# Optimization experiments

Measured on AMD Instinct MI355X. Metric: run time of the kernel, lower is better.

The kernel has to match this reference:

```python
import jax, jax.numpy as jnp
import numpy as np

DIM = 512
L = 4096
B, H, W = 8, 64, 64
EPS = 1e-06
BN_EPS = 1e-05


def setup_inputs() -> dict:
    key = jax.random.key(0)
    ks = jax.random.split(key, 16)
    s = 1.0 / np.sqrt(DIM)
    d = {
        'x': jax.random.normal(ks[0], (B, DIM, H, W), dtype=jnp.float32),
        'pos_emb': jax.random.normal(ks[1], (1, L, DIM), dtype=jnp.float32),
        'Wq': jax.random.uniform(ks[2], (DIM, DIM), jnp.float32, -s, s),
        'bq': jax.random.uniform(ks[3], (DIM,), jnp.float32, -s, s),
        'Wk': jax.random.uniform(ks[4], (DIM, DIM), jnp.float32, -s, s),
        'bk': jax.random.uniform(ks[5], (DIM,), jnp.float32, -s, s),
        'Wv': jax.random.uniform(ks[6], (DIM, DIM), jnp.float32, -s, s),
        'bv': jax.random.uniform(ks[7], (DIM,), jnp.float32, -s, s),
        'Wq1': jax.random.uniform(ks[8], (DIM, DIM), jnp.float32, -s, s),
        'bq1': jax.random.uniform(ks[9], (DIM,), jnp.float32, -s, s),
        'Wk1': jax.random.uniform(ks[10], (DIM, DIM), jnp.float32, -s, s),
        'bk1': jax.random.uniform(ks[11], (DIM,), jnp.float32, -s, s),
        'gamma': jax.random.normal(ks[12], (1,), jnp.float32) * 0.1,
        'bn_weight': jnp.ones((DIM,), jnp.float32),
        'bn_bias': jnp.zeros((DIM,), jnp.float32),
    }
    return d


def reference(x, pos_emb, Wq, bq, Wk, bk, Wv, bv, Wq1, bq1, Wk1, bk1, gamma, bn_weight, bn_bias):
    Bb, C, Hh, Ww = x.shape
    # [B,C,H,W] -> [B, L, C] tokens
    xs = x.transpose(0, 2, 3, 1).reshape(Bb, Hh * Ww, C) + pos_emb
    Q = jax.nn.relu(xs @ Wq.T + bq)   # kernel_fun = ReLU
    K = jax.nn.relu(xs @ Wk.T + bk)
    V = xs @ Wv.T + bv
    Q1 = xs @ Wq1.T + bq1
    K1 = xs @ Wk1.T + bk1
    # torch einsum 'blc,bcc,bl->blc' uses only diag(KV); compute it directly:
    # diagKV[b,c] = sum_l K[b,l,c] * V[b,l,c]
    diagKV = jnp.einsum('blc,blc->bc', K, V)
    Ksum = K.sum(axis=1)  # == K^T summed over last axis, [B,C]
    Z = 1.0 / jnp.einsum('blc,bc->bl', Q, Ksum + EPS)
    result = Q * diagKV[:, None, :] * Z[:, :, None]  # [B,L,C]
    # channel-softmax attention: softmax over last dim of Q1^T @ K1, [B,C,C]
    mid = jax.nn.softmax(jnp.einsum('blc,bld->bcd', Q1, K1), axis=-1)
    result = result @ mid  # [B,L,C]
    xs = xs + gamma * result
    y = xs.transpose(0, 2, 1).reshape(Bb, C, Hh, Ww)
    # BatchNorm2d in training mode (fresh module): batch stats, biased variance
    mean = y.mean(axis=(0, 2, 3))
    var = y.var(axis=(0, 2, 3))
    yn = (y - mean[None, :, None, None]) * jax.lax.rsqrt(var + BN_EPS)[None, :, None, None]
    yn = yn * bn_weight[None, :, None, None] + bn_bias[None, :, None, None]
    return jax.nn.relu(yn)
```

## Files before the change

### kernel.cpp

```cpp
#include <hip/hip_runtime.h>
#include <stdint.h>

typedef float f32x4 __attribute__((ext_vector_type(4)));
typedef short bf16x8 __attribute__((ext_vector_type(8)));

__device__ __forceinline__ float bf2f(unsigned short h){
  union { unsigned int u; float f; } v; v.u = ((unsigned int)h) << 16; return v.f;
}
__device__ __forceinline__ unsigned short f2bf(float f){
  union { float f; unsigned int u; } v; v.f = f;
  return (unsigned short)((v.u + 0x7fffu + ((v.u >> 16) & 1u)) >> 16);
}

typedef __attribute__((address_space(1))) const unsigned int ga_u32;
typedef __attribute__((address_space(3))) unsigned int ls_u32;
__device__ __forceinline__ void async_load16(const void* g, void* l){
  __builtin_amdgcn_global_load_lds((ga_u32*)g, (ls_u32*)l, 16, 0, 0);
}

#define CFENCE() asm volatile("" ::: "memory")
#define SB0() __builtin_amdgcn_sched_barrier(0)

__global__ __launch_bounds__(256) void k_prep_w(
    const float* __restrict__ w0, const float* __restrict__ w1,
    const float* __restrict__ w2, const float* __restrict__ w3,
    const float* __restrict__ w4, unsigned short* __restrict__ out)
{
  int i = blockIdx.x * 256 + threadIdx.x;
  const float* w = (blockIdx.y == 0) ? w0 : (blockIdx.y == 1) ? w1 :
                   (blockIdx.y == 2) ? w2 : (blockIdx.y == 3) ? w3 : w4;
  out[(size_t)blockIdx.y * 262144 + i] = f2bf(w[i]);
}
__global__ __launch_bounds__(256) void k_prep_b(
    const float* __restrict__ b0, const float* __restrict__ b1,
    const float* __restrict__ b2, const float* __restrict__ b3,
    const float* __restrict__ b4, float* __restrict__ out)
{
  int i = blockIdx.x * 256 + threadIdx.x;
  int s = i >> 9, r = i & 511;
  const float* b = (s == 0) ? b0 : (s == 1) ? b1 : (s == 2) ? b2 : (s == 3) ? b3 : b4;
  out[i] = b[r];
}

__global__ __launch_bounds__(256) void k_build_xs(
    const float* __restrict__ x, const float* __restrict__ pos,
    unsigned short* __restrict__ xsb)
{
  __shared__ float tile[64][65];
  const int lt = blockIdx.x, ct = blockIdx.y;
  const int t = threadIdx.x;
  const int rr = t >> 3, c8 = (t & 7) * 8;
  float pr[16];
  #pragma unroll
  for (int pass = 0; pass < 2; pass++){
    int gl = lt*64 + rr + pass*32;
    f32x4 p0 = *(const f32x4*)(pos + (size_t)gl * 512 + ct*64 + c8);
    f32x4 p1 = *(const f32x4*)(pos + (size_t)gl * 512 + ct*64 + c8 + 4);
    #pragma unroll
    for (int s = 0; s < 4; s++){ pr[pass*8+s] = p0[s]; pr[pass*8+4+s] = p1[s]; }
  }
  for (int b = 0; b < 8; b++){
    #pragma unroll
    for (int pass = 0; pass < 2; pass++){
      int r = rr + pass * 32;
      const float* src = x + ((size_t)b * 512 + ct*64 + r) * 4096 + lt*64 + c8;
      f32x4 v0 = *(const f32x4*)src;
      f32x4 v1 = *(const f32x4*)(src + 4);
      #pragma unroll
      for (int s = 0; s < 4; s++){ tile[r][c8+s] = v0[s]; tile[r][c8+4+s] = v1[s]; }
    }
    __syncthreads();
    #pragma unroll
    for (int pass = 0; pass < 2; pass++){
      int ll = rr + pass * 32;
      int gl = lt*64 + ll;
      bf16x8 hv;
      #pragma unroll
      for (int s = 0; s < 8; s++)
        hv[s] = (short)f2bf(tile[c8+s][ll] + pr[pass*8+s]);
      *(bf16x8*)(xsb + ((size_t)b * 4096 + gl) * 512 + ct*64 + c8) = hv;
    }
    __syncthreads();
  }
}

__global__ __launch_bounds__(256) void k_softmax_t(
    const float* __restrict__ S0, const float* __restrict__ S1,
    const float* __restrict__ diag, unsigned short* __restrict__ midT)
{
  __shared__ unsigned short tr[64 * 514];
  const int it = blockIdx.x, z = blockIdx.y;
  const int t = threadIdx.x;
  const int lane = t & 63, w = t >> 6;
  for (int rr = 0; rr < 16; rr++){
    int i = rr*4 + w;
    size_t rowo = (size_t)z * 262144 + (size_t)(it*64 + i) * 512 + lane*8;
    const float* p0 = S0 + rowo;
    const float* p1 = S1 + rowo;
    f32x4 v0 = *(const f32x4*)p0 + *(const f32x4*)p1;
    f32x4 v1 = *(const f32x4*)(p0 + 4) + *(const f32x4*)(p1 + 4);
    float mx = v0[0];
    #pragma unroll
    for (int s = 1; s < 4; s++) mx = fmaxf(mx, v0[s]);
    #pragma unroll
    for (int s = 0; s < 4; s++) mx = fmaxf(mx, v1[s]);
    #pragma unroll
    for (int m = 1; m < 64; m <<= 1) mx = fmaxf(mx, __shfl_xor(mx, m));
    float e[8]; float sum = 0.f;
    #pragma unroll
    for (int s = 0; s < 4; s++){ e[s]   = __expf(v0[s] - mx); sum += e[s]; }
    #pragma unroll
    for (int s = 0; s < 4; s++){ e[4+s] = __expf(v1[s] - mx); sum += e[4+s]; }
    #pragma unroll
    for (int m = 1; m < 64; m <<= 1) sum += __shfl_xor(sum, m);
    float sc = diag[z*512 + it*64 + i] / sum;
    #pragma unroll
    for (int s = 0; s < 8; s++) tr[i*514 + lane*8 + s] = f2bf(e[s] * sc);
  }
  __syncthreads();
  for (int ps = 0; ps < 16; ps++){
    int j = ps*32 + (t >> 3);
    int i0 = (t & 7) * 8;
    bf16x8 hv;
    #pragma unroll
    for (int s = 0; s < 8; s++) hv[s] = (short)tr[(i0+s)*514 + j];
    *(bf16x8*)(midT + ((size_t)z*512 + j)*512 + it*64 + i0) = hv;
  }
}

#define GEMM_PRE()                                                            \
  const int tid = threadIdx.x;                                                \
  const int lane = tid & 63;                                                  \
  const int wave = tid >> 6;                                                  \
  const int wm = wave >> 1, wn = wave & 1;                                    \
  size_t aoff[4], boff[4]; int ldsq[4];                                       \
  _Pragma("unroll")                                                           \
  for (int i = 0; i < 4; i++){                                                \
    int qq = i*4 + wave;                                                      \
    int ch = qq*64 + lane;                                                    \
    int m  = ch >> 3, p = ch & 7;                                             \
    int lc = p ^ (m & 7);                                                     \
    aoff[i] = (size_t)(m0 + m) * K + lc*8;                                    \
    boff[i] = (size_t)m * K + lc*8;                                           \
    ldsq[i] = qq * 1024;                                                      \
  }                                                                           \
  f32x4 acc[4][4];                                                            \
  const f32x4 vzero = {0.f,0.f,0.f,0.f};                                      \
  _Pragma("unroll")                                                           \
  for (int i = 0; i < 4; i++)                                                 \
    _Pragma("unroll")                                                         \
    for (int j = 0; j < 4; j++) acc[i][j] = vzero;                            \
  int arow[4], brow[4];                                                       \
  _Pragma("unroll")                                                           \
  for (int f = 0; f < 4; f++){                                                \
    arow[f] = (wm*64 + f*16 + (lane & 15)) * 64;                              \
    brow[f] = (wn*64 + f*16 + (lane & 15)) * 64;                              \
  }                                                                           \
  const int kg = lane >> 4;                                                   \
  const int l7 = lane & 7;                                                    \
  const int l15 = lane & 15;

#define GEMM_STAGE2(buf, kt, BB)                                              \
  _Pragma("unroll")                                                           \
  for (int i = 0; i < 4; i++){                                                \
    async_load16(Ae + aoff[i] + (kt)*64, (char*)&smem[(buf)*8192] + ldsq[i]); \
    async_load16((BB) + boff[i] + (kt)*64, (char*)&smem[16384 + (buf)*8192] + ldsq[i]); \
  }

#define GEMM_COMPUTE2(buf, ACC)                                               \
  _Pragma("unroll")                                                           \
  for (int ks = 0; ks < 2; ks++){                                             \
    bf16x8 a[4], b[4];                                                        \
    const int pa = (ks*4 + kg) ^ l7;                                          \
    _Pragma("unroll")                                                         \
    for (int f = 0; f < 4; f++){                                              \
      a[f] = *(const bf16x8*)&smem[(buf)*8192 + arow[f] + pa*8];              \
      b[f] = *(const bf16x8*)&smem[16384 + (buf)*8192 + brow[f] + pa*8];      \
    }                                                                         \
    _Pragma("unroll")                                                         \
    for (int i = 0; i < 4; i++)                                               \
      _Pragma("unroll")                                                       \
      for (int j = 0; j < 4; j++)                                             \
        (ACC)[i][j] = __builtin_amdgcn_mfma_f32_16x16x32_bf16(a[i], b[j], (ACC)[i][j], 0, 0, 0); \
  }

#define GEMM_KLOOP2(nkt, BB)                                                  \
  GEMM_STAGE2(0, 0, BB);                                                      \
  __syncthreads();                                                            \
  { int cur = 0;                                                              \
    for (int kt = 0; kt < (nkt); kt++){                                       \
      if (kt + 1 < (nkt)) { GEMM_STAGE2(cur ^ 1, kt + 1, BB); }               \
      GEMM_COMPUTE2(cur, acc);                                                \
      __syncthreads();                                                        \
      cur ^= 1;                                                               \
    } }

__global__ __launch_bounds__(256) void gemm_mid(
    const unsigned short* __restrict__ A,
    const unsigned short* __restrict__ Bt,
    float* __restrict__ out0, float* __restrict__ out1)
{
  __shared__ unsigned short smem[32768];
  const int bid = blockIdx.x;
  const int wgid = (bid & 7) * 32 + (bid >> 3);
  const int part = wgid & 1;
  const int ntile = (wgid >> 1) & 3;
  const int mtile = (wgid >> 3) & 3;
  const int z = wgid >> 5;
  const int m0 = mtile * 128, n0 = ntile * 128;
  const int K = 4096;
  const unsigned short* Ae = A  + (size_t)z * 2097152 + part * 2048;
  const unsigned short* Be = Bt + (size_t)z * 2097152 + part * 2048 + (size_t)n0 * 4096;

  GEMM_PRE();
  GEMM_KLOOP2(32, Be);

  float* outf = part ? out1 : out0;
  #pragma unroll
  for (int j = 0; j < 4; j++){
    int cidx = n0 + wn*64 + j*16 + l15;
    #pragma unroll
    for (int i = 0; i < 4; i++){
      int r = m0 + wm*64 + i*16 + kg*4;
      #pragma unroll
      for (int q = 0; q < 4; q++)
        outf[(size_t)z * 262144 + (size_t)(r + q) * 512 + cidx] = acc[i][j][q];
    }
  }
}

__global__ __launch_bounds__(256, 2) void gemm_proj2(
    const unsigned short* __restrict__ A,
    const unsigned short* __restrict__ W,
    const float* __restrict__ bias5,
    unsigned short* __restrict__ Qb,
    unsigned short* __restrict__ Q1T, unsigned short* __restrict__ K1T,
    float* __restrict__ diag, float* __restrict__ ksum)
{
  __shared__ unsigned short smem[32768];
  const int bid = blockIdx.x;
  const int wgid = (bid & 7) * 512 + (bid >> 3);
  const int mtile = wgid >> 4;
  const int unit  = wgid & 15;
  const int m0 = mtile * 128;
  const int K = 512;
  const unsigned short* Ae = A;

  int mode, cb;
  const unsigned short* BeK; const unsigned short* BeV = W;
  if (unit < 4)      { mode = 0; cb = unit*128;      BeK = W + (size_t)cb * 512; }
  else if (unit < 8) { mode = 1; cb = (unit-4)*128;  BeK = W + 262144 + (size_t)cb * 512;
                                                     BeV = W + 524288 + (size_t)cb * 512; }
  else if (unit < 12){ mode = 2; cb = (unit-8)*128;  BeK = W + 786432 + (size_t)cb * 512; }
  else               { mode = 3; cb = (unit-12)*128; BeK = W + 1048576 + (size_t)cb * 512; }

  GEMM_PRE();

  if (mode == 1){
    const int bz = mtile >> 5;
    GEMM_STAGE2(0, 0, BeK);
    __syncthreads();
    int cur = 0;
    for (int kt = 0; kt < 8; kt++){
      if (kt < 7) { GEMM_STAGE2(cur ^ 1, kt + 1, BeK); }
      else        { GEMM_STAGE2(cur ^ 1, 0, BeV); }
      GEMM_COMPUTE2(cur, acc);
      __syncthreads();
      cur ^= 1;
    }
    GEMM_STAGE2(cur ^ 1, 1, BeV);
    unsigned int kpk[4][4][2];
    #pragma unroll
    for (int j = 0; j < 4; j++){
      const int cj = cb + wn*64 + j*16 + l15;
      const float bb = bias5[512 + cj];
      float ks_ = 0.f;
      #pragma unroll
      for (int i = 0; i < 4; i++){
        #pragma unroll
        for (int h = 0; h < 2; h++){
          float v0 = acc[i][j][2*h]   + bb; v0 = v0 > 0.f ? v0 : 0.f;
          float v1 = acc[i][j][2*h+1] + bb; v1 = v1 > 0.f ? v1 : 0.f;
          unsigned short h0 = f2bf(v0), h1 = f2bf(v1);
          kpk[i][j][h] = (unsigned)h0 | ((unsigned)h1 << 16);
          ks_ += bf2f(h0) + bf2f(h1);
        }
        acc[i][j] = vzero;
      }
      ks_ += __shfl_xor(ks_, 16);
      ks_ += __shfl_xor(ks_, 32);
      if (lane < 16) atomicAdd(&ksum[bz*512 + cj], ks_);
    }
    for (int kt = 0; kt < 8; kt++){
      if (kt >= 1 && kt < 7) { GEMM_STAGE2(cur ^ 1, kt + 1, BeV); }
      GEMM_COMPUTE2(cur, acc);
      __syncthreads();
      cur ^= 1;
    }
    #pragma unroll
    for (int j = 0; j < 4; j++){
      const int cj = cb + wn*64 + j*16 + l15;
      const float bb = bias5[1024 + cj];
      float dv = 0.f;
      #pragma unroll
      for (int i = 0; i < 4; i++){
        #pragma unroll
        for (int h = 0; h < 2; h++){
          float v0 = bf2f(f2bf(acc[i][j][2*h]   + bb));
          float v1 = bf2f(f2bf(acc[i][j][2*h+1] + bb));
          dv += bf2f((unsigned short)(kpk[i][j][h] & 0xffffu)) * v0
              + bf2f((unsigned short)(kpk[i][j][h] >> 16))     * v1;
        }
      }
      dv += __shfl_xor(dv, 16);
      dv += __shfl_xor(dv, 32);
      if (lane < 16) atomicAdd(&diag[bz*512 + cj], dv);
    }
    return;
  }

  GEMM_KLOOP2(8, BeK);

  if (mode == 0){
    #pragma unroll
    for (int j = 0; j < 4; j++){
      const int cl = wn*64 + j*16 + l15;
      const float bb = bias5[cb + cl];
      #pragma unroll
      for (int i = 0; i < 4; i++){
        const int rb = wm*64 + i*16 + kg*4;
        #pragma unroll
        for (int q = 0; q < 4; q++){
          float v = acc[i][j][q] + bb; v = v > 0.f ? v : 0.f;
          smem[(rb + q)*136 + cl] = f2bf(v);
        }
      }
    }
    __syncthreads();
    #pragma unroll
    for (int rep = 0; rep < 8; rep++){
      const int rl = rep*16 + (tid >> 4);
      const int c0 = (tid & 15) * 8;
      bf16x8 v = *(const bf16x8*)&smem[rl*136 + c0];
      *(bf16x8*)(Qb + (size_t)(m0 + rl) * 512 + cb + c0) = v;
    }
  } else {
    unsigned short* o = (mode == 2) ? Q1T : K1T;
    const int bz = mtile >> 5;
    const int l0 = (mtile & 31) * 128;
    const int bco = (mode == 2) ? 1536 : 2048;
    #pragma unroll
    for (int j = 0; j < 4; j++){
      const int cl = wn*64 + j*16 + l15;
      const float bb = bias5[bco + cb + cl];
      #pragma unroll
      for (int i = 0; i < 4; i++){
        const int lb = wm*64 + i*16 + kg*4;
        #pragma unroll
        for (int q = 0; q < 4; q++)
          smem[cl*136 + lb + q] = f2bf(acc[i][j][q] + bb);
      }
    }
    __syncthreads();
    #pragma unroll
    for (int rep = 0; rep < 8; rep++){
      const int cl = rep*16 + (tid >> 4);
      const int lch = tid & 15;
      bf16x8 v = *(const bf16x8*)&smem[cl*136 + lch*8];
      *(bf16x8*)(o + ((size_t)bz*512 + cb + cl)*4096 + l0 + lch*8) = v;
    }
  }
}

#define G8_PRE(AE)                                                            \
  const int t = threadIdx.x;                                                  \
  const int lane = t & 63;                                                    \
  const int wave = t >> 6;                                                    \
  const int wm = wave >> 2, wn = wave & 3;                                    \
  const int l15 = lane & 15, kg = lane >> 4;                                  \
  const int l7 = lane & 7;                                                    \
  const int lcw = ((t & 7) ^ ((t >> 3) & 7)) * 8;                             \
  const unsigned short* a_src = (AE) + (size_t)(m0 + (t >> 3)) * 512 + lcw;   \
  f32x4 acc[8][4];                                                            \
  const f32x4 vzero = {0.f,0.f,0.f,0.f};                                      \
  _Pragma("unroll")                                                           \
  for (int i = 0; i < 8; i++)                                                 \
    _Pragma("unroll")                                                         \
    for (int j = 0; j < 4; j++) acc[i][j] = vzero;                            \
  bf16x8 af[4][2], bf[4][2];

#define STAGE_A(D,H,TT) do{                                                   \
  async_load16(a_src + (H)*65536 + (TT)*64,                                   \
               (char*)smem + ((D)*16384 + (H)*8192 + t*8)*2);                 \
  async_load16(a_src + (H)*65536 + 32768 + (TT)*64,                           \
               (char*)smem + ((D)*16384 + (H)*8192 + 4096 + t*8)*2);          \
}while(0)

#define STAGE_B(D,H,TT) do{                                                   \
  async_load16(b_src + (H)*65536 + (TT)*64,                                   \
               (char*)smem + (32768 + (D)*16384 + (H)*8192 + t*8)*2);         \
  async_load16(b_src + (H)*65536 + 32768 + (TT)*64,                           \
               (char*)smem + (32768 + (D)*16384 + (H)*8192 + 4096 + t*8)*2);  \
}while(0)

#define READ_A(D, MH) do{                                                     \
  _Pragma("unroll")                                                           \
  for (int mfl = 0; mfl < 4; ++mfl){                                          \
    const int rl = ((MH)*4 + mfl)*16 + l15;                                   \
    _Pragma("unroll")                                                         \
    for (int ks = 0; ks < 2; ++ks){                                           \
      const int ck = (ks*4 + kg) ^ (rl & 7);                                  \
      af[mfl][ks] = *(const bf16x8*)&smem[(D)*16384 + wm*8192 + rl*64 + ck*8];\
    }                                                                         \
  }                                                                           \
}while(0)

#define READ_B(D, NP) do{                                                     \
  _Pragma("unroll")                                                           \
  for (int nfl = 0; nfl < 2; ++nfl){                                          \
    const int nf = (NP)*2 + nfl;                                              \
    const int rbl = (wn & 1)*64 + nf*16 + l15;                                \
    _Pragma("unroll")                                                         \
    for (int ks = 0; ks < 2; ++ks){                                           \
      const int ck = (ks*4 + kg) ^ (rbl & 7);                                 \
      bf[nf][ks] = *(const bf16x8*)&smem[32768 + (D)*16384 + (wn>>1)*8192 + rbl*64 + ck*8]; \
    }                                                                         \
  }                                                                           \
}while(0)

#define ZDOT(KT, MH) do{ if ((wave & 3) == 0){                                \
  _Pragma("unroll")                                                           \
  for (int ks = 0; ks < 2; ++ks){                                             \
    const int ck = (ks*4 + kg) ^ l7;                                          \
    f32x4 ka = *(const f32x4*)&kse[(KT)*64 + ck*8];                           \
    f32x4 kb = *(const f32x4*)&kse[(KT)*64 + ck*8 + 4];                       \
    _Pragma("unroll")                                                         \
    for (int mfl = 0; mfl < 4; ++mfl){                                        \
      _Pragma("unroll")                                                       \
      for (int jj = 0; jj < 4; ++jj)                                          \
        zacc[(MH)*4+mfl] += bf2f((unsigned short)af[mfl][ks][jj])   * ka[jj]  \
                          + bf2f((unsigned short)af[mfl][ks][4+jj]) * kb[jj]; \
    }                                                                         \
  } } }while(0)

#define QUAD(MH, NP)                                                          \
  _Pragma("unroll")                                                           \
  for (int mfl = 0; mfl < 4; ++mfl)                                           \
    _Pragma("unroll")                                                         \
    for (int nfl = 0; nfl < 2; ++nfl)                                         \
      _Pragma("unroll")                                                       \
      for (int ks = 0; ks < 2; ++ks)                                          \
        acc[(MH)*4+mfl][(NP)*2+nfl] = __builtin_amdgcn_mfma_f32_16x16x32_bf16(\
            af[mfl][ks], bf[(NP)*2+nfl][ks], acc[(MH)*4+mfl][(NP)*2+nfl], 0,0,0);

#define PH_MID()  CFENCE(); __builtin_amdgcn_s_barrier();                     \
  __builtin_amdgcn_s_setprio(1); SB0()
#define PH_END()  SB0(); __builtin_amdgcn_s_setprio(0); CFENCE();             \
  __builtin_amdgcn_s_barrier(); CFENCE()
#define PH_END_VM4() SB0(); __builtin_amdgcn_s_setprio(0);                    \
  asm volatile("s_waitcnt vmcnt(4)" ::: "memory");                            \
  __builtin_amdgcn_s_barrier(); CFENCE()
#define PH_END_VM0() SB0(); __builtin_amdgcn_s_setprio(0);                    \
  asm volatile("s_waitcnt vmcnt(0)" ::: "memory");                            \
  __builtin_amdgcn_s_barrier(); CFENCE()

#define G8_KLOOP_Z()                                                          \
  STAGE_A(0,0,0); STAGE_A(0,1,0); STAGE_B(0,0,0); STAGE_B(0,1,0);             \
  STAGE_B(1,0,1); STAGE_B(1,1,1);                                             \
  asm volatile("s_waitcnt vmcnt(4)" ::: "memory");                            \
  __builtin_amdgcn_s_barrier(); CFENCE();                                     \
  for (int it = 0; it < 3; ++it){                                             \
    const int t1 = 2*it + 1, t2 = 2*it + 2, t3 = 2*it + 3;                    \
    READ_A(0,0); ZDOT(2*it,0); READ_B(0,0); STAGE_A(1,0,t1);                  \
    PH_MID(); QUAD(0,0); PH_END();                                            \
    READ_B(0,1); STAGE_A(1,1,t1);                                             \
    PH_MID(); QUAD(0,1); PH_END();                                            \
    READ_A(0,1); ZDOT(2*it,1); STAGE_B(0,0,t2);                               \
    PH_MID(); QUAD(1,0); PH_END();                                            \
    STAGE_A(0,0,t2);                                                          \
    PH_MID(); QUAD(1,1); PH_END_VM4();                                        \
    READ_A(1,0); ZDOT(2*it+1,0); READ_B(1,0); STAGE_A(0,1,t2);                \
    PH_MID(); QUAD(0,0); PH_END();                                            \
    READ_B(1,1); STAGE_B(0,1,t2);                                             \
    PH_MID(); QUAD(0,1); PH_END();                                            \
    READ_A(1,1); ZDOT(2*it+1,1); STAGE_B(1,0,t3);                             \
    PH_MID(); QUAD(1,0); PH_END();                                            \
    STAGE_B(1,1,t3);                                                          \
    PH_MID(); QUAD(1,1); PH_END_VM4();                                        \
  }                                                                           \
  { READ_A(0,0); ZDOT(6,0); READ_B(0,0); STAGE_A(1,0,7);                      \
    PH_MID(); QUAD(0,0); PH_END();                                            \
    READ_B(0,1); STAGE_A(1,1,7);                                              \
    PH_MID(); QUAD(0,1); PH_END();                                            \
    READ_A(0,1); ZDOT(6,1);                                                   \
    PH_MID(); QUAD(1,0); PH_END();                                            \
    PH_MID(); QUAD(1,1); PH_END_VM0();                                        \
    READ_A(1,0); ZDOT(7,0); READ_B(1,0);                                      \
    PH_MID(); QUAD(0,0); PH_END();                                            \
    READ_B(1,1);                                                              \
    PH_MID(); QUAD(0,1); PH_END();                                            \
    READ_A(1,1); ZDOT(7,1);                                                   \
    PH_MID(); QUAD(1,0); PH_END();                                            \
    PH_MID(); QUAD(1,1); PH_END(); }

__global__ __launch_bounds__(512, 2) void gemm8_res(
    const unsigned short* __restrict__ A,
    const unsigned short* __restrict__ Bt,
    const float* __restrict__ ksum,
    unsigned short* __restrict__ outh,
    const float* __restrict__ gamma_p,
    float* __restrict__ bnS, float* __restrict__ bnQ)
{
  __shared__ unsigned short smem[65536];
  __shared__ float kse[512];
  __shared__ float zlds[256];
  const int bid = blockIdx.x;
  const int wgid = (bid & 7) * 32 + (bid >> 3);
  const int mtile = wgid >> 1;
  const int ntile = wgid & 1;
  const int m0 = mtile * 256;
  const int nc0 = ntile * 256;
  const int bz = mtile >> 4;

  G8_PRE(A);
  const unsigned short* b_src =
      Bt + (size_t)bz * 262144 + (size_t)(nc0 + (t >> 3)) * 512 + lcw;
  float zacc[8] = {0.f,0.f,0.f,0.f,0.f,0.f,0.f,0.f};
  kse[t & 511] = ksum[bz*512 + (t & 511)] + 1e-6f;
  __syncthreads();

  G8_KLOOP_Z();

  if ((wave & 3) == 0){
    #pragma unroll
    for (int r8 = 0; r8 < 8; r8++){
      float zz = zacc[r8];
      zz += __shfl_xor(zz, 16);
      zz += __shfl_xor(zz, 32);
      if (kg == 0) zlds[wm*128 + r8*16 + l15] = 1.0f / zz;
    }
  }
  const float g = gamma_p[0];
  __syncthreads();
  #pragma unroll
  for (int nf = 0; nf < 4; nf++){
    int cl = wn*64 + nf*16 + l15;
    #pragma unroll
    for (int mf = 0; mf < 8; mf++){
      int rbase = wm*128 + mf*16 + kg*4;
      #pragma unroll
      for (int q = 0; q < 4; q++){
        int rl = rbase + q;
        smem[rl*256 + (cl ^ (((rl >> 2) & 3) << 4))] =
            f2bf(g * zlds[rl] * acc[mf][nf][q]);
      }
    }
  }
  __syncthreads();
  float sc[8] = {0.f,0.f,0.f,0.f,0.f,0.f,0.f,0.f};
  float sq[8] = {0.f,0.f,0.f,0.f,0.f,0.f,0.f,0.f};
  const int c0 = (t & 31) * 8;
  #pragma unroll
  for (int rep = 0; rep < 16; rep++){
    int rl = rep*16 + (t >> 5);
    bf16x8 ga = *(const bf16x8*)&smem[rl*256 + (c0 ^ (((rl >> 2) & 3) << 4))];
    size_t gidx = (size_t)(m0 + rl) * 512 + nc0 + c0;
    bf16x8 xv = *(const bf16x8*)(outh + gidx);
    bf16x8 yv;
    #pragma unroll
    for (int j = 0; j < 8; j++){
      float y = bf2f((unsigned short)xv[j]) + bf2f((unsigned short)ga[j]);
      yv[j] = (short)f2bf(y);
      sc[j] += y; sq[j] += y * y;
    }
    *(bf16x8*)(outh + gidx) = yv;
  }
  __syncthreads();
  float* red = (float*)(void*)smem;
  const int tg = t >> 5;
  f32x4 s0 = {sc[0],sc[1],sc[2],sc[3]}, s1 = {sc[4],sc[5],sc[6],sc[7]};
  f32x4 q0 = {sq[0],sq[1],sq[2],sq[3]}, q1 = {sq[4],sq[5],sq[6],sq[7]};
  *(f32x4*)&red[tg*256 + c0]        = s0;  *(f32x4*)&red[tg*256 + c0 + 4]        = s1;
  *(f32x4*)&red[4096 + tg*256 + c0] = q0;  *(f32x4*)&red[4096 + tg*256 + c0 + 4] = q1;
  __syncthreads();
  if (t < 256){
    float ss = 0.f, qq = 0.f;
    #pragma unroll
    for (int gg = 0; gg < 16; gg++){
      ss += red[gg*256 + t];
      qq += red[4096 + gg*256 + t];
    }
    atomicAdd(&bnS[nc0 + t], ss);
    atomicAdd(&bnQ[nc0 + t], qq);
  }
}

__global__ __launch_bounds__(256) void k_bn_finalize(
    const unsigned short* __restrict__ y, const float* __restrict__ bnS,
    const float* __restrict__ bnQ, const float* __restrict__ bnw,
    const float* __restrict__ bnb, float* __restrict__ out)
{
  __shared__ float tile[64][65];
  __shared__ float scale_s[64], shift_s[64];
  const int lt = blockIdx.x, ct = blockIdx.y, b = blockIdx.z;
  const int t = threadIdx.x;
  if (t < 64){
    int c = ct*64 + t;
    float s = bnS[c], q = bnQ[c];
    float mean = s * (1.0f / 32768.0f);
    float var  = q * (1.0f / 32768.0f) - mean * mean;
    float inv  = rsqrtf(var + 1e-5f);
    float scv  = bnw[c] * inv;
    scale_s[t] = scv;
    shift_s[t] = bnb[c] - mean * scv;
  }
  const int rr = t >> 3, c8 = (t & 7) * 8;
  #pragma unroll
  for (int pass = 0; pass < 2; pass++){
    int l = rr + pass * 32;
    bf16x8 v = *(const bf16x8*)(y + ((size_t)b * 4096 + lt*64 + l) * 512 + ct*64 + c8);
    #pragma unroll
    for (int s = 0; s < 8; s++) tile[l][c8+s] = bf2f((unsigned short)v[s]);
  }
  __syncthreads();
  #pragma unroll
  for (int pass = 0; pass < 2; pass++){
    int c = rr + pass * 32;
    float scv = scale_s[c], sh = shift_s[c];
    f32x4 o0, o1;
    #pragma unroll
    for (int s = 0; s < 4; s++){
      float v = tile[c8+s][c] * scv + sh;     o0[s] = v > 0.f ? v : 0.f;
      float w = tile[c8+4+s][c] * scv + sh;   o1[s] = w > 0.f ? w : 0.f;
    }
    float* dp = out + ((size_t)b * 512 + ct*64 + c) * 4096 + lt*64 + c8;
    *(f32x4*)dp = o0;
    *(f32x4*)(dp + 4) = o1;
  }
}

extern "C" void kernel_launch(void* const* d_in, const int* in_sizes, int n_in,
                              void* d_out, int out_size, void* d_ws, size_t ws_size,
                              hipStream_t stream)
{
  const float* x    = (const float*)d_in[0];
  const float* pos  = (const float*)d_in[1];
  const float* Wq   = (const float*)d_in[2];
  const float* bq   = (const float*)d_in[3];
  const float* Wk   = (const float*)d_in[4];
  const float* bk   = (const float*)d_in[5];
  const float* Wv   = (const float*)d_in[6];
  const float* bv   = (const float*)d_in[7];
  const float* Wq1  = (const float*)d_in[8];
  const float* bq1  = (const float*)d_in[9];
  const float* Wk1  = (const float*)d_in[10];
  const float* bk1  = (const float*)d_in[11];
  const float* gam  = (const float*)d_in[12];
  const float* bnw  = (const float*)d_in[13];
  const float* bnb  = (const float*)d_in[14];
  float* out = (float*)d_out;
  char* ws = (char*)d_ws;

  const size_t MB = 1ull << 20;
  const size_t OFF_XSB  = 0;
  const size_t OFF_QB   = 32*MB;
  const size_t OFF_Q1T  = 64*MB;
  const size_t OFF_K1T  = 96*MB;
  const size_t OFF_SF0  = 128*MB;
  const size_t OFF_SF1  = 136*MB;
  const size_t OFF_MIDT = 144*MB;
  const size_t OFF_WBF  = 148*MB;
  const size_t OFF_B5   = 151*MB;
  const size_t OFF_DIAG = 152*MB;
  const size_t OFF_KSUM = OFF_DIAG + 16384;
  const size_t OFF_BNS  = OFF_KSUM + 16384;
  const size_t OFF_BNQ  = OFF_BNS + 2048;
  const size_t WS_NEED  = OFF_BNQ + 2048;
  if (ws_size < WS_NEED) return;

  unsigned short* xsb  = (unsigned short*)(ws + OFF_XSB);
  unsigned short* Qb   = (unsigned short*)(ws + OFF_QB);
  unsigned short* Q1T  = (unsigned short*)(ws + OFF_Q1T);
  unsigned short* K1T  = (unsigned short*)(ws + OFF_K1T);
  float*          Sf0  = (float*)(ws + OFF_SF0);
  float*          Sf1  = (float*)(ws + OFF_SF1);
  unsigned short* midT = (unsigned short*)(ws + OFF_MIDT);
  unsigned short* wbf  = (unsigned short*)(ws + OFF_WBF);
  float* bias5 = (float*)(ws + OFF_B5);
  float* diag = (float*)(ws + OFF_DIAG);
  float* ksum = (float*)(ws + OFF_KSUM);
  float* bnS  = (float*)(ws + OFF_BNS);
  float* bnQ  = (float*)(ws + OFF_BNQ);

  hipMemsetAsync(ws + OFF_DIAG, 0, 16384 + 16384 + 2048 + 2048, stream);

  k_prep_w  <<<dim3(1024, 5), 256, 0, stream>>>(Wq, Wk, Wv, Wq1, Wk1, wbf);
  k_prep_b  <<<dim3(10),      256, 0, stream>>>(bq, bk, bv, bq1, bk1, bias5);
  k_build_xs<<<dim3(64, 8),   256, 0, stream>>>(x, pos, xsb);

  gemm_proj2<<<dim3(4096), 256, 0, stream>>>(xsb, wbf, bias5, Qb, Q1T, K1T, diag, ksum);

  gemm_mid<<<dim3(256), 256, 0, stream>>>(Q1T, K1T, Sf0, Sf1);

  k_softmax_t<<<dim3(8, 8), 256, 0, stream>>>(Sf0, Sf1, diag, midT);

  gemm8_res<<<dim3(256), 512, 0, stream>>>(Qb, midT, ksum, xsb, gam, bnS, bnQ);

  k_bn_finalize<<<dim3(64, 8, 8), 256, 0, stream>>>(xsb, bnS, bnQ, bnw, bnb, out);
}
```

Baseline: 257.7 us.

## Compute channel attention via Gram matrix of xs instead of Q1/K1 projections

Replaces the Q1 and K1 projections with an algebraic factorisation: S = Wq1 (xs^T xs) Wk1^T plus bias corrections built from column sums of xs. This removes half of the projection GEMM work and the transposed Q1/K1 writes. In their place it adds a 512x512 Gram GEMM over L per batch, two small GEMMs, a transposed xs copy, and several small kernels (colsum, u/w vectors, combine, Z, softmax, transpose-scale). The normaliser Z also moves out of the main GEMM into its own kernel. The cost is many more launches, extra global traffic, and a different bf16 rounding path for S.

```diff
diff --git a/kernel.cpp b/kernel.cpp
--- a/kernel.cpp
+++ b/kernel.cpp
@@ -44,87 +44,185 @@
 
 __global__ __launch_bounds__(256) void k_build_xs(
     const float* __restrict__ x, const float* __restrict__ pos,
-    unsigned short* __restrict__ xsb)
+    unsigned short* __restrict__ xsb, unsigned short* __restrict__ xsT)
 {
   __shared__ float tile[64][65];
-  const int lt = blockIdx.x, ct = blockIdx.y;
+  __shared__ unsigned short tile2[64][72];
+  const int lt = blockIdx.x, ct = blockIdx.y, b = blockIdx.z;
   const int t = threadIdx.x;
   const int rr = t >> 3, c8 = (t & 7) * 8;
-  float pr[16];
   #pragma unroll
   for (int pass = 0; pass < 2; pass++){
-    int gl = lt*64 + rr + pass*32;
-    f32x4 p0 = *(const f32x4*)(pos + (size_t)gl * 512 + ct*64 + c8);
-    f32x4 p1 = *(const f32x4*)(pos + (size_t)gl * 512 + ct*64 + c8 + 4);
-    #pragma unroll
-    for (int s = 0; s < 4; s++){ pr[pass*8+s] = p0[s]; pr[pass*8+4+s] = p1[s]; }
-  }
-  for (int b = 0; b < 8; b++){
-    #pragma unroll
-    for (int pass = 0; pass < 2; pass++){
-      int r = rr + pass * 32;
-      const float* src = x + ((size_t)b * 512 + ct*64 + r) * 4096 + lt*64 + c8;
-      f32x4 v0 = *(const f32x4*)src;
-      f32x4 v1 = *(const f32x4*)(src + 4);
+    int r = rr + pass * 32;
+    const float* src = x + ((size_t)b * 512 + ct*64 + r) * 4096 + lt*64 + c8;
+    f32x4 v0 = *(const f32x4*)src;
+    f32x4 v1 = *(const f32x4*)(src + 4);
+    #pragma unroll
+    for (int s = 0; s < 4; s++){ tile[r][c8+s] = v0[s]; tile[r][c8+4+s] = v1[s]; }
+  }
+  __syncthreads();
+  #pragma unroll
+  for (int pass = 0; pass < 2; pass++){
+    int ll = rr + pass * 32;
+    int gl = lt*64 + ll;
+    const float* pp = pos + (size_t)gl * 512 + ct*64 + c8;
+    bf16x8 hv;
+    #pragma unroll
+    for (int s = 0; s < 8; s++){
+      unsigned short h = f2bf(tile[c8+s][ll] + pp[s]);
+      hv[s] = (short)h;
+      tile2[c8+s][ll] = h;
+    }
+    *(bf16x8*)(xsb + ((size_t)b * 4096 + gl) * 512 + ct*64 + c8) = hv;
+  }
+  __syncthreads();
+  #pragma unroll
+  for (int rep = 0; rep < 2; rep++){
+    int c = rep*32 + (t >> 3);
+    int l0 = (t & 7) * 8;
+    bf16x8 v = *(const bf16x8*)&tile2[c][l0];
+    *(bf16x8*)(xsT + ((size_t)b * 512 + ct*64 + c) * 4096 + lt*64 + l0) = v;
+  }
+}
+
+__global__ __launch_bounds__(256) void k_colsum(
+    const unsigned short* __restrict__ xsT, float* __restrict__ svec)
+{
+  const int cblk = blockIdx.x, b = blockIdx.y;
+  const int t = threadIdx.x;
+  const int wave = t >> 6, lane = t & 63;
+  for (int rr = 0; rr < 16; rr++){
+    int c = cblk*64 + wave*16 + rr;
+    const unsigned short* row = xsT + ((size_t)b * 512 + c) * 4096;
+    float a[8] = {0.f,0.f,0.f,0.f,0.f,0.f,0.f,0.f};
+    #pragma unroll
+    for (int pass = 0; pass < 8; pass++){
+      bf16x8 v = *(const bf16x8*)(row + pass*512 + lane*8);
       #pragma unroll
-      for (int s = 0; s < 4; s++){ tile[r][c8+s] = v0[s]; tile[r][c8+4+s] = v1[s]; }
-    }
-    __syncthreads();
-    #pragma unroll
-    for (int pass = 0; pass < 2; pass++){
-      int ll = rr + pass * 32;
-      int gl = lt*64 + ll;
-      bf16x8 hv;
+      for (int j = 0; j < 8; j++) a[j] += bf2f((unsigned short)v[j]);
+    }
+    float sum = a[0]+a[1]+a[2]+a[3]+a[4]+a[5]+a[6]+a[7];
+    #pragma unroll
+    for (int m = 1; m < 64; m <<= 1) sum += __shfl_xor(sum, m);
+    if (lane == 0) svec[b*512 + c] = sum;
+  }
+}
+
+__global__ __launch_bounds__(256) void k_uw(
+    const unsigned short* __restrict__ wbf, const float* __restrict__ svec,
+    float* __restrict__ u, float* __restrict__ w)
+{
+  __shared__ float sv[512];
+  const int sel = blockIdx.x, b = blockIdx.y;
+  const int t = threadIdx.x;
+  sv[t] = svec[b*512 + t]; sv[t+256] = svec[b*512 + t + 256];
+  __syncthreads();
+  const unsigned short* Wp = wbf + (size_t)(3 + sel) * 262144;
+  float* o = sel ? w : u;
+  #pragma unroll
+  for (int rep = 0; rep < 2; rep++){
+    int e = rep*256 + t;
+    const unsigned short* row = Wp + (size_t)e * 512;
+    float acc = 0.f;
+    for (int ch = 0; ch < 64; ch++){
+      bf16x8 v = *(const bf16x8*)(row + ch*8);
       #pragma unroll
-      for (int s = 0; s < 8; s++)
-        hv[s] = (short)f2bf(tile[c8+s][ll] + pr[pass*8+s]);
-      *(bf16x8*)(xsb + ((size_t)b * 4096 + gl) * 512 + ct*64 + c8) = hv;
-    }
-    __syncthreads();
-  }
-}
-
-__global__ __launch_bounds__(256) void k_softmax_t(
-    const float* __restrict__ S0, const float* __restrict__ S1,
-    const float* __restrict__ diag, unsigned short* __restrict__ midT)
-{
-  __shared__ unsigned short tr[64 * 514];
-  const int it = blockIdx.x, z = blockIdx.y;
+      for (int j = 0; j < 8; j++) acc += bf2f((unsigned short)v[j]) * sv[ch*8+j];
+    }
+    o[b*512 + e] = acc;
+  }
+}
+
+__global__ __launch_bounds__(256) void k_combineG(
+    const float* __restrict__ g0, const float* __restrict__ g1,
+    unsigned short* __restrict__ gb)
+{
+  size_t i8 = ((size_t)blockIdx.x * 256 + threadIdx.x) * 8;
+  f32x4 a0 = *(const f32x4*)(g0 + i8)     + *(const f32x4*)(g1 + i8);
+  f32x4 a1 = *(const f32x4*)(g0 + i8 + 4) + *(const f32x4*)(g1 + i8 + 4);
+  bf16x8 hv;
+  #pragma unroll
+  for (int s = 0; s < 4; s++){ hv[s] = (short)f2bf(a0[s]); hv[4+s] = (short)f2bf(a1[s]); }
+  *(bf16x8*)(gb + i8) = hv;
+}
+
+__global__ __launch_bounds__(256) void k_z(
+    const unsigned short* __restrict__ Qb, const float* __restrict__ ksum,
+    float* __restrict__ Z)
+{
+  const int row = blockIdx.x * 4 + (threadIdx.x >> 6);
+  const int lane = threadIdx.x & 63;
+  const int b = row >> 12;
+  bf16x8 q = *(const bf16x8*)(Qb + (size_t)row * 512 + lane * 8);
+  f32x4 k0 = *(const f32x4*)(ksum + b*512 + lane*8);
+  f32x4 k1 = *(const f32x4*)(ksum + b*512 + lane*8 + 4);
+  float den = 0.f;
+  #pragma unroll
+  for (int s = 0; s < 4; s++) den += bf2f((unsigned short)q[s])   * (k0[s] + 1e-6f);
+  #pragma unroll
+  for (int s = 0; s < 4; s++) den += bf2f((unsigned short)q[4+s]) * (k1[s] + 1e-6f);
+  #pragma unroll
+  for (int m = 1; m < 64; m <<= 1) den += __shfl_xor(den, m);
+  if (lane == 0) Z[row] = 1.0f / den;
+}
+
+__global__ __launch_bounds__(64) void k_softmax(
+    const float* __restrict__ S, unsigned short* __restrict__ mid)
+{
+  const size_t row = blockIdx.x;
+  const int lane = threadIdx.x;
+  const float* p = S + row * 512 + lane * 8;
+  f32x4 v0 = *(const f32x4*)p, v1 = *(const f32x4*)(p + 4);
+  float mx = v0[0];
+  #pragma unroll
+  for (int s = 1; s < 4; s++) mx = fmaxf(mx, v0[s]);
+  #pragma unroll
+  for (int s = 0; s < 4; s++) mx = fmaxf(mx, v1[s]);
+  #pragma unroll
+  for (int m = 1; m < 64; m <<= 1) mx = fmaxf(mx, __shfl_xor(mx, m));
+  float e[8]; float sum = 0.f;
+  #pragma unroll
+  for (int s = 0; s < 4; s++){ e[s]   = __expf(v0[s] - mx); sum += e[s]; }
+  #pragma unroll
+  for (int s = 0; s < 4; s++){ e[4+s] = __expf(v1[s] - mx); sum += e[4+s]; }
+  #pragma unroll
+  for (int m = 1; m < 64; m <<= 1) sum += __shfl_xor(sum, m);
+  float inv = 1.0f / sum;
+  bf16x8 hv;
+  #pragma unroll
+  for (int s = 0; s < 8; s++) hv[s] = (short)f2bf(e[s] * inv);
+  *(bf16x8*)(mid + row * 512 + lane * 8) = hv;
+}
+
+__global__ __launch_bounds__(256) void k_transpose_scale(
+    const unsigned short* __restrict__ in, const float* __restrict__ diag,
+    unsigned short* __restrict__ out)
+{
+  __shared__ float tile[64][65];
+  const int rt = blockIdx.x, ct = blockIdx.y, z = blockIdx.z;
+  const unsigned short* src = in  + (size_t)z * 262144;
+  unsigned short*       dst = out + (size_t)z * 262144;
   const int t = threadIdx.x;
-  const int lane = t & 63, w = t >> 6;
-  for (int rr = 0; rr < 16; rr++){
-    int i = rr*4 + w;
-    size_t rowo = (size_t)z * 262144 + (size_t)(it*64 + i) * 512 + lane*8;
-    const float* p0 = S0 + rowo;
-    const float* p1 = S1 + rowo;
-    f32x4 v0 = *(const f32x4*)p0 + *(const f32x4*)p1;
-    f32x4 v1 = *(const f32x4*)(p0 + 4) + *(const f32x4*)(p1 + 4);
-    float mx = v0[0];
-    #pragma unroll
-    for (int s = 1; s < 4; s++) mx = fmaxf(mx, v0[s]);
-    #pragma unroll
-    for (int s = 0; s < 4; s++) mx = fmaxf(mx, v1[s]);
-    #pragma unroll
-    for (int m = 1; m < 64; m <<= 1) mx = fmaxf(mx, __shfl_xor(mx, m));
-    float e[8]; float sum = 0.f;
-    #pragma unroll
-    for (int s = 0; s < 4; s++){ e[s]   = __expf(v0[s] - mx); sum += e[s]; }
-    #pragma unroll
-    for (int s = 0; s < 4; s++){ e[4+s] = __expf(v1[s] - mx); sum += e[4+s]; }
-    #pragma unroll
-    for (int m = 1; m < 64; m <<= 1) sum += __shfl_xor(sum, m);
-    float sc = diag[z*512 + it*64 + i] / sum;
-    #pragma unroll
-    for (int s = 0; s < 8; s++) tr[i*514 + lane*8 + s] = f2bf(e[s] * sc);
-  }
-  __syncthreads();
-  for (int ps = 0; ps < 16; ps++){
-    int j = ps*32 + (t >> 3);
-    int i0 = (t & 7) * 8;
+  const int rr = t >> 3, c8 = (t & 7) * 8;
+  #pragma unroll
+  for (int pass = 0; pass < 2; pass++){
+    int r = rr + pass * 32;
+    bf16x8 v = *(const bf16x8*)(src + (size_t)(rt*64 + r) * 512 + ct*64 + c8);
+    #pragma unroll
+    for (int s = 0; s < 8; s++) tile[r][c8+s] = bf2f((unsigned short)v[s]);
+  }
+  __syncthreads();
+  f32x4 dg0 = *(const f32x4*)(diag + z*512 + rt*64 + c8);
+  f32x4 dg1 = *(const f32x4*)(diag + z*512 + rt*64 + c8 + 4);
+  #pragma unroll
+  for (int pass = 0; pass < 2; pass++){
+    int c = rr + pass * 32;
     bf16x8 hv;
     #pragma unroll
-    for (int s = 0; s < 8; s++) hv[s] = (short)tr[(i0+s)*514 + j];
-    *(bf16x8*)(midT + ((size_t)z*512 + j)*512 + it*64 + i0) = hv;
+    for (int s = 0; s < 4; s++) hv[s]   = (short)f2bf(tile[c8+s][c]   * dg0[s]);
+    #pragma unroll
+    for (int s = 0; s < 4; s++) hv[4+s] = (short)f2bf(tile[c8+4+s][c] * dg1[s]);
+    *(bf16x8*)(dst + (size_t)(ct*64 + c) * 512 + rt*64 + c8) = hv;
   }
 }
 
@@ -195,9 +293,8 @@
       cur ^= 1;                                                               \
     } }
 
-__global__ __launch_bounds__(256) void gemm_mid(
+__global__ __launch_bounds__(256) void gemm_G(
     const unsigned short* __restrict__ A,
-    const unsigned short* __restrict__ Bt,
     float* __restrict__ out0, float* __restrict__ out1)
 {
   __shared__ unsigned short smem[32768];
@@ -209,8 +306,8 @@
   const int z = wgid >> 5;
   const int m0 = mtile * 128, n0 = ntile * 128;
   const int K = 4096;
-  const unsigned short* Ae = A  + (size_t)z * 2097152 + part * 2048;
-  const unsigned short* Be = Bt + (size_t)z * 2097152 + part * 2048 + (size_t)n0 * 4096;
+  const unsigned short* Ae = A + (size_t)z * 2097152 + part * 2048;
+  const unsigned short* Be = Ae + (size_t)n0 * 4096;
 
   GEMM_PRE();
   GEMM_KLOOP2(32, Be);
@@ -229,30 +326,106 @@
   }
 }
 
+__global__ __launch_bounds__(256) void gemm_P(
+    const unsigned short* __restrict__ Wq1b,
+    const unsigned short* __restrict__ Gb,
+    unsigned short* __restrict__ P)
+{
+  __shared__ unsigned short smem[32768];
+  const int bid = blockIdx.x;
+  const int wgid = (bid & 7) * 16 + (bid >> 3);
+  const int z = wgid >> 4;
+  const int mtile = (wgid >> 2) & 3, ntile = wgid & 3;
+  const int m0 = mtile * 128, n0 = ntile * 128;
+  const int K = 512;
+  const unsigned short* Ae = Wq1b;
+  const unsigned short* Be = Gb + (size_t)z * 262144 + (size_t)n0 * 512;
+
+  GEMM_PRE();
+  GEMM_KLOOP2(8, Be);
+
+  #pragma unroll
+  for (int j = 0; j < 4; j++){
+    const int cl = wn*64 + j*16 + l15;
+    #pragma unroll
+    for (int i = 0; i < 4; i++){
+      const int rb = wm*64 + i*16 + kg*4;
+      #pragma unroll
+      for (int q = 0; q < 4; q++)
+        smem[(rb + q)*136 + cl] = f2bf(acc[i][j][q]);
+    }
+  }
+  __syncthreads();
+  #pragma unroll
+  for (int rep = 0; rep < 8; rep++){
+    const int rl = rep*16 + (tid >> 4);
+    const int c0 = (tid & 15) * 8;
+    bf16x8 v = *(const bf16x8*)&smem[rl*136 + c0];
+    *(bf16x8*)(P + (size_t)z * 262144 + (size_t)(m0 + rl) * 512 + n0 + c0) = v;
+  }
+}
+
+__global__ __launch_bounds__(256) void gemm_S(
+    const unsigned short* __restrict__ P,
+    const unsigned short* __restrict__ Wk1b,
+    const float* __restrict__ bias5,
+    const float* __restrict__ u, const float* __restrict__ w,
+    float* __restrict__ Sf)
+{
+  __shared__ unsigned short smem[32768];
+  const int bid = blockIdx.x;
+  const int wgid = (bid & 7) * 16 + (bid >> 3);
+  const int z = wgid >> 4;
+  const int mtile = (wgid >> 2) & 3, ntile = wgid & 3;
+  const int m0 = mtile * 128, n0 = ntile * 128;
+  const int K = 512;
+  const unsigned short* Ae = P + (size_t)z * 262144;
+  const unsigned short* Be = Wk1b + (size_t)n0 * 512;
+
+  GEMM_PRE();
+  GEMM_KLOOP2(8, Be);
+
+  #pragma unroll
+  for (int j = 0; j < 4; j++){
+    int cd = n0 + wn*64 + j*16 + l15;
+    float bkv = bias5[2048 + cd];
+    float wv  = w[z*512 + cd] + 4096.0f * bkv;
+    #pragma unroll
+    for (int i = 0; i < 4; i++){
+      int r = m0 + wm*64 + i*16 + kg*4;
+      #pragma unroll
+      for (int q = 0; q < 4; q++){
+        int rr = r + q;
+        float uq  = u[z*512 + rr];
+        float bqv = bias5[1536 + rr];
+        Sf[(size_t)z * 262144 + (size_t)rr * 512 + cd] =
+            acc[i][j][q] + uq * bkv + bqv * wv;
+      }
+    }
+  }
+}
+
 __global__ __launch_bounds__(256, 2) void gemm_proj2(
     const unsigned short* __restrict__ A,
     const unsigned short* __restrict__ W,
     const float* __restrict__ bias5,
     unsigned short* __restrict__ Qb,
-    unsigned short* __restrict__ Q1T, unsigned short* __restrict__ K1T,
     float* __restrict__ diag, float* __restrict__ ksum)
 {
   __shared__ unsigned short smem[32768];
   const int bid = blockIdx.x;
-  const int wgid = (bid & 7) * 512 + (bid >> 3);
-  const int mtile = wgid >> 4;
-  const int unit  = wgid & 15;
+  const int wgid = (bid & 7) * 256 + (bid >> 3);
+  const int mtile = wgid >> 3;
+  const int unit  = wgid & 7;
   const int m0 = mtile * 128;
   const int K = 512;
   const unsigned short* Ae = A;
 
   int mode, cb;
   const unsigned short* BeK; const unsigned short* BeV = W;
-  if (unit < 4)      { mode = 0; cb = unit*128;      BeK = W + (size_t)cb * 512; }
-  else if (unit < 8) { mode = 1; cb = (unit-4)*128;  BeK = W + 262144 + (size_t)cb * 512;
-                                                     BeV = W + 524288 + (size_t)cb * 512; }
-  else if (unit < 12){ mode = 2; cb = (unit-8)*128;  BeK = W + 786432 + (size_t)cb * 512; }
-  else               { mode = 3; cb = (unit-12)*128; BeK = W + 1048576 + (size_t)cb * 512; }
+  if (unit < 4){ mode = 0; cb = unit*128;     BeK = W + (size_t)cb * 512; }
+  else         { mode = 1; cb = (unit-4)*128; BeK = W + 262144 + (size_t)cb * 512;
+                                              BeV = W + 524288 + (size_t)cb * 512; }
 
   GEMM_PRE();
 
@@ -321,54 +494,27 @@
 
   GEMM_KLOOP2(8, BeK);
 
-  if (mode == 0){
-    #pragma unroll
-    for (int j = 0; j < 4; j++){
-      const int cl = wn*64 + j*16 + l15;
-      const float bb = bias5[cb + cl];
+  #pragma unroll
+  for (int j = 0; j < 4; j++){
+    const int cl = wn*64 + j*16 + l15;
+    const float bb = bias5[cb + cl];
+    #pragma unroll
+    for (int i = 0; i < 4; i++){
+      const int rb = wm*64 + i*16 + kg*4;
       #pragma unroll
-      for (int i = 0; i < 4; i++){
-        const int rb = wm*64 + i*16 + kg*4;
-        #pragma unroll
-        for (int q = 0; q < 4; q++){
-          float v = acc[i][j][q] + bb; v = v > 0.f ? v : 0.f;
-          smem[(rb + q)*136 + cl] = f2bf(v);
-        }
+      for (int q = 0; q < 4; q++){
+        float v = acc[i][j][q] + bb; v = v > 0.f ? v : 0.f;
+        smem[(rb + q)*136 + cl] = f2bf(v);
       }
     }
-    __syncthreads();
-    #pragma unroll
-    for (int rep = 0; rep < 8; rep++){
-      const int rl = rep*16 + (tid >> 4);
-      const int c0 = (tid & 15) * 8;
-      bf16x8 v = *(const bf16x8*)&smem[rl*136 + c0];
-      *(bf16x8*)(Qb + (size_t)(m0 + rl) * 512 + cb + c0) = v;
-    }
-  } else {
-    unsigned short* o = (mode == 2) ? Q1T : K1T;
-    const int bz = mtile >> 5;
-    const int l0 = (mtile & 31) * 128;
-    const int bco = (mode == 2) ? 1536 : 2048;
-    #pragma unroll
-    for (int j = 0; j < 4; j++){
-      const int cl = wn*64 + j*16 + l15;
-      const float bb = bias5[bco + cb + cl];
-      #pragma unroll
-      for (int i = 0; i < 4; i++){
-        const int lb = wm*64 + i*16 + kg*4;
-        #pragma unroll
-        for (int q = 0; q < 4; q++)
-          smem[cl*136 + lb + q] = f2bf(acc[i][j][q] + bb);
-      }
-    }
-    __syncthreads();
-    #pragma unroll
-    for (int rep = 0; rep < 8; rep++){
-      const int cl = rep*16 + (tid >> 4);
-      const int lch = tid & 15;
-      bf16x8 v = *(const bf16x8*)&smem[cl*136 + lch*8];
-      *(bf16x8*)(o + ((size_t)bz*512 + cb + cl)*4096 + l0 + lch*8) = v;
-    }
+  }
+  __syncthreads();
+  #pragma unroll
+  for (int rep = 0; rep < 8; rep++){
+    const int rl = rep*16 + (tid >> 4);
+    const int c0 = (tid & 15) * 8;
+    bf16x8 v = *(const bf16x8*)&smem[rl*136 + c0];
+    *(bf16x8*)(Qb + (size_t)(m0 + rl) * 512 + cb + c0) = v;
   }
 }
 
@@ -378,7 +524,6 @@
   const int wave = t >> 6;                                                    \
   const int wm = wave >> 2, wn = wave & 3;                                    \
   const int l15 = lane & 15, kg = lane >> 4;                                  \
-  const int l7 = lane & 7;                                                    \
   const int lcw = ((t & 7) ^ ((t >> 3) & 7)) * 8;                             \
   const unsigned short* a_src = (AE) + (size_t)(m0 + (t >> 3)) * 512 + lcw;   \
   f32x4 acc[8][4];                                                            \
@@ -428,21 +573,6 @@
   }                                                                           \
 }while(0)
 
-#define ZDOT(KT, MH) do{ if ((wave & 3) == 0){                                \
-  _Pragma("unroll")                                                           \
-  for (int ks = 0; ks < 2; ++ks){                                             \
-    const int ck = (ks*4 + kg) ^ l7;                                          \
-    f32x4 ka = *(const f32x4*)&kse[(KT)*64 + ck*8];                           \
-    f32x4 kb = *(const f32x4*)&kse[(KT)*64 + ck*8 + 4];                       \
-    _Pragma("unroll")                                                         \
-    for (int mfl = 0; mfl < 4; ++mfl){                                        \
-      _Pragma("unroll")                                                       \
-      for (int jj = 0; jj < 4; ++jj)                                          \
-        zacc[(MH)*4+mfl] += bf2f((unsigned short)af[mfl][ks][jj])   * ka[jj]  \
-                          + bf2f((unsigned short)af[mfl][ks][4+jj]) * kb[jj]; \
-    }                                                                         \
-  } } }while(0)
-
 #define QUAD(MH, NP)                                                          \
   _Pragma("unroll")                                                           \
   for (int mfl = 0; mfl < 4; ++mfl)                                           \
@@ -464,83 +594,71 @@
   asm volatile("s_waitcnt vmcnt(0)" ::: "memory");                            \
   __builtin_amdgcn_s_barrier(); CFENCE()
 
-#define G8_KLOOP_Z()                                                          \
+#define G8_KLOOP()                                                            \
   STAGE_A(0,0,0); STAGE_A(0,1,0); STAGE_B(0,0,0); STAGE_B(0,1,0);             \
   STAGE_B(1,0,1); STAGE_B(1,1,1);                                             \
   asm volatile("s_waitcnt vmcnt(4)" ::: "memory");                            \
   __builtin_amdgcn_s_barrier(); CFENCE();                                     \
   for (int it = 0; it < 3; ++it){                                             \
     const int t1 = 2*it + 1, t2 = 2*it + 2, t3 = 2*it + 3;                    \
-    READ_A(0,0); ZDOT(2*it,0); READ_B(0,0); STAGE_A(1,0,t1);                  \
+    READ_A(0,0); READ_B(0,0); STAGE_A(1,0,t1);                                \
     PH_MID(); QUAD(0,0); PH_END();                                            \
     READ_B(0,1); STAGE_A(1,1,t1);                                             \
     PH_MID(); QUAD(0,1); PH_END();                                            \
-    READ_A(0,1); ZDOT(2*it,1); STAGE_B(0,0,t2);                               \
+    READ_A(0,1); STAGE_B(0,0,t2);                                             \
     PH_MID(); QUAD(1,0); PH_END();                                            \
     STAGE_A(0,0,t2);                                                          \
     PH_MID(); QUAD(1,1); PH_END_VM4();                                        \
-    READ_A(1,0); ZDOT(2*it+1,0); READ_B(1,0); STAGE_A(0,1,t2);                \
+    READ_A(1,0); READ_B(1,0); STAGE_A(0,1,t2);                                \
     PH_MID(); QUAD(0,0); PH_END();                                            \
     READ_B(1,1); STAGE_B(0,1,t2);                                             \
     PH_MID(); QUAD(0,1); PH_END();                                            \
-    READ_A(1,1); ZDOT(2*it+1,1); STAGE_B(1,0,t3);                             \
+    READ_A(1,1); STAGE_B(1,0,t3);                                             \
     PH_MID(); QUAD(1,0); PH_END();                                            \
     STAGE_B(1,1,t3);                                                          \
     PH_MID(); QUAD(1,1); PH_END_VM4();                                        \
   }                                                                           \
-  { READ_A(0,0); ZDOT(6,0); READ_B(0,0); STAGE_A(1,0,7);                      \
+  { READ_A(0,0); READ_B(0,0); STAGE_A(1,0,7);                                 \
     PH_MID(); QUAD(0,0); PH_END();                                            \
     READ_B(0,1); STAGE_A(1,1,7);                                              \
     PH_MID(); QUAD(0,1); PH_END();                                            \
-    READ_A(0,1); ZDOT(6,1);                                                   \
+    READ_A(0,1);                                                              \
     PH_MID(); QUAD(1,0); PH_END();                                            \
     PH_MID(); QUAD(1,1); PH_END_VM0();                                        \
-    READ_A(1,0); ZDOT(7,0); READ_B(1,0);                                      \
+    READ_A(1,0); READ_B(1,0);                                                 \
     PH_MID(); QUAD(0,0); PH_END();                                            \
     READ_B(1,1);                                                              \
     PH_MID(); QUAD(0,1); PH_END();                                            \
-    READ_A(1,1); ZDOT(7,1);                                                   \
+    READ_A(1,1);                                                              \
     PH_MID(); QUAD(1,0); PH_END();                                            \
     PH_MID(); QUAD(1,1); PH_END(); }
 
 __global__ __launch_bounds__(512, 2) void gemm8_res(
     const unsigned short* __restrict__ A,
     const unsigned short* __restrict__ Bt,
-    const float* __restrict__ ksum,
+    const float* __restrict__ Zp,
     unsigned short* __restrict__ outh,
     const float* __restrict__ gamma_p,
     float* __restrict__ bnS, float* __restrict__ bnQ)
 {
   __shared__ unsigned short smem[65536];
-  __shared__ float kse[512];
-  __shared__ float zlds[256];
+  __shared__ float zbuf[256];
   const int bid = blockIdx.x;
   const int wgid = (bid & 7) * 32 + (bid >> 3);
   const int mtile = wgid >> 1;
   const int ntile = wgid & 1;
   const int m0 = mtile * 256;
   const int nc0 = ntile * 256;
-  const int bz = mtile >> 4;
 
   G8_PRE(A);
   const unsigned short* b_src =
-      Bt + (size_t)bz * 262144 + (size_t)(nc0 + (t >> 3)) * 512 + lcw;
-  float zacc[8] = {0.f,0.f,0.f,0.f,0.f,0.f,0.f,0.f};
-  kse[t & 511] = ksum[bz*512 + (t & 511)] + 1e-6f;
-  __syncthreads();
-
-  G8_KLOOP_Z();
-
-  if ((wave & 3) == 0){
-    #pragma unroll
-    for (int r8 = 0; r8 < 8; r8++){
-      float zz = zacc[r8];
-      zz += __shfl_xor(zz, 16);
-      zz += __shfl_xor(zz, 32);
-      if (kg == 0) zlds[wm*128 + r8*16 + l15] = 1.0f / zz;
-    }
-  }
+      Bt + (size_t)(mtile >> 4) * 262144 + (size_t)(nc0 + (t >> 3)) * 512 + lcw;
+
+  G8_KLOOP();
+
   const float g = gamma_p[0];
+  __syncthreads();
+  if (t < 256) zbuf[t] = Zp[m0 + t];
   __syncthreads();
   #pragma unroll
   for (int nf = 0; nf < 4; nf++){
@@ -552,7 +670,7 @@
       for (int q = 0; q < 4; q++){
         int rl = rbase + q;
         smem[rl*256 + (cl ^ (((rl >> 2) & 3) << 4))] =
-            f2bf(g * zlds[rl] * acc[mf][nf][q]);
+            f2bf(g * zbuf[rl] * acc[mf][nf][q]);
       }
     }
   }
@@ -664,14 +782,21 @@
   const size_t MB = 1ull << 20;
   const size_t OFF_XSB  = 0;
   const size_t OFF_QB   = 32*MB;
-  const size_t OFF_Q1T  = 64*MB;
-  const size_t OFF_K1T  = 96*MB;
-  const size_t OFF_SF0  = 128*MB;
-  const size_t OFF_SF1  = 136*MB;
-  const size_t OFF_MIDT = 144*MB;
-  const size_t OFF_WBF  = 148*MB;
-  const size_t OFF_B5   = 151*MB;
-  const size_t OFF_DIAG = 152*MB;
+  const size_t OFF_XST  = 64*MB;
+  const size_t OFF_GP0  = 96*MB;
+  const size_t OFF_GP1  = 104*MB;
+  const size_t OFF_GBF  = 112*MB;
+  const size_t OFF_PBF  = 116*MB;
+  const size_t OFF_SF   = 120*MB;
+  const size_t OFF_MIDB = 128*MB;
+  const size_t OFF_MIDT = 132*MB;
+  const size_t OFF_WBF  = 136*MB;
+  const size_t OFF_B5   = 139*MB;
+  const size_t OFF_SV   = 140*MB;
+  const size_t OFF_UV   = OFF_SV + 16384;
+  const size_t OFF_WV   = OFF_UV + 16384;
+  const size_t OFF_Z    = 141*MB;
+  const size_t OFF_DIAG = 142*MB;
   const size_t OFF_KSUM = OFF_DIAG + 16384;
   const size_t OFF_BNS  = OFF_KSUM + 16384;
   const size_t OFF_BNQ  = OFF_BNS + 2048;
@@ -680,13 +805,20 @@
 
   unsigned short* xsb  = (unsigned short*)(ws + OFF_XSB);
   unsigned short* Qb   = (unsigned short*)(ws + OFF_QB);
-  unsigned short* Q1T  = (unsigned short*)(ws + OFF_Q1T);
-  unsigned short* K1T  = (unsigned short*)(ws + OFF_K1T);
-  float*          Sf0  = (float*)(ws + OFF_SF0);
-  float*          Sf1  = (float*)(ws + OFF_SF1);
+  unsigned short* xsT  = (unsigned short*)(ws + OFF_XST);
+  float*          Gp0  = (float*)(ws + OFF_GP0);
+  float*          Gp1  = (float*)(ws + OFF_GP1);
+  unsigned short* Gbf  = (unsigned short*)(ws + OFF_GBF);
+  unsigned short* Pbf  = (unsigned short*)(ws + OFF_PBF);
+  float*          Sf   = (float*)(ws + OFF_SF);
+  unsigned short* midb = (unsigned short*)(ws + OFF_MIDB);
   unsigned short* midT = (unsigned short*)(ws + OFF_MIDT);
   unsigned short* wbf  = (unsigned short*)(ws + OFF_WBF);
   float* bias5 = (float*)(ws + OFF_B5);
+  float* svec = (float*)(ws + OFF_SV);
+  float* uvec = (float*)(ws + OFF_UV);
+  float* wvec = (float*)(ws + OFF_WV);
+  float* Zp   = (float*)(ws + OFF_Z);
   float* diag = (float*)(ws + OFF_DIAG);
   float* ksum = (float*)(ws + OFF_KSUM);
   float* bnS  = (float*)(ws + OFF_BNS);
@@ -696,15 +828,25 @@
 
   k_prep_w  <<<dim3(1024, 5), 256, 0, stream>>>(Wq, Wk, Wv, Wq1, Wk1, wbf);
   k_prep_b  <<<dim3(10),      256, 0, stream>>>(bq, bk, bv, bq1, bk1, bias5);
-  k_build_xs<<<dim3(64, 8),   256, 0, stream>>>(x, pos, xsb);
-
-  gemm_proj2<<<dim3(4096), 256, 0, stream>>>(xsb, wbf, bias5, Qb, Q1T, K1T, diag, ksum);
-
-  gemm_mid<<<dim3(256), 256, 0, stream>>>(Q1T, K1T, Sf0, Sf1);
-
-  k_softmax_t<<<dim3(8, 8), 256, 0, stream>>>(Sf0, Sf1, diag, midT);
-
-  gemm8_res<<<dim3(256), 512, 0, stream>>>(Qb, midT, ksum, xsb, gam, bnS, bnQ);
+  k_build_xs<<<dim3(64, 8, 8),256, 0, stream>>>(x, pos, xsb, xsT);
+
+  gemm_proj2<<<dim3(2048), 256, 0, stream>>>(xsb, wbf, bias5, Qb, diag, ksum);
+
+  k_colsum<<<dim3(8, 8), 256, 0, stream>>>(xsT, svec);
+  k_uw    <<<dim3(2, 8), 256, 0, stream>>>(wbf, svec, uvec, wvec);
+
+  gemm_G    <<<dim3(256),  256, 0, stream>>>(xsT, Gp0, Gp1);
+  k_combineG<<<dim3(1024), 256, 0, stream>>>(Gp0, Gp1, Gbf);
+
+  gemm_P<<<dim3(128), 256, 0, stream>>>(wbf + 3*262144, Gbf, Pbf);
+  gemm_S<<<dim3(128), 256, 0, stream>>>(Pbf, wbf + 4*262144, bias5, uvec, wvec, Sf);
+
+  k_z<<<dim3(8192), 256, 0, stream>>>(Qb, ksum, Zp);
+
+  k_softmax<<<dim3(4096), 64, 0, stream>>>(Sf, midb);
+  k_transpose_scale<<<dim3(8, 8, 8), 256, 0, stream>>>(midb, diag, midT);
+
+  gemm8_res<<<dim3(256), 512, 0, stream>>>(Qb, midT, Zp, xsb, gam, bnS, bnQ);
 
   k_bn_finalize<<<dim3(64, 8, 8), 256, 0, stream>>>(xsb, bnS, bnQ, bnw, bnb, out);
 }
```

Measured after the change: 263.1 us. 2.1% more time.
